# Kernel tuning notes

Measured on AMD Instinct MI355X. Metric: run time of the kernel, lower is better.

Reference implementation:

```python
import jax, jax.numpy as jnp
import numpy as np
import math

DIM = 1024
MLP = 4096
D_STATE = 16
D_CONV = 4
EXPAND = 2
D_INNER = EXPAND * DIM
HALF = D_INNER // 2
DT_RANK = math.ceil(DIM / 16)
BSZ = 2
SEQ = 2048
LN_EPS = 1e-5


def setup_inputs() -> dict:
    key = jax.random.key(0)
    ks = jax.random.split(key, 12)
    s = lambda k, shape, sc: jax.random.normal(k, shape, dtype=jnp.float32) * sc
    return {
        "x": s(ks[0], (BSZ, SEQ, DIM), 1.0),
        "ln1_g": jnp.ones((DIM,), jnp.float32),
        "ln1_b": jnp.zeros((DIM,), jnp.float32),
        "in_proj_w": s(ks[1], (D_INNER, DIM), 0.02),
        "conv_x_w": s(ks[2], (HALF, 1, D_CONV), 0.1),
        "conv_x_b": jnp.zeros((HALF,), jnp.float32),
        "conv_z_w": s(ks[3], (HALF, 1, D_CONV), 0.1),
        "conv_z_b": jnp.zeros((HALF,), jnp.float32),
        "x_proj_w": s(ks[4], (DT_RANK + 2 * D_STATE, HALF), 0.02),
        "dt_proj_w": s(ks[5], (HALF, DT_RANK), 0.02),
        "dt_proj_b": s(ks[6], (HALF,), 0.1),
        "A_log": jnp.log(jnp.tile(jnp.arange(1, D_STATE + 1, dtype=jnp.float32), (HALF, 1))),
        "Dp": jnp.ones((HALF,), jnp.float32),
        "out_proj_w": s(ks[7], (DIM, D_INNER), 0.02),
        "ln2_g": jnp.ones((DIM,), jnp.float32),
        "ln2_b": jnp.zeros((DIM,), jnp.float32),
        "mlp_w1": s(ks[8], (MLP, DIM), 0.02),
        "mlp_b1": jnp.zeros((MLP,), jnp.float32),
        "mlp_w2": s(ks[9], (DIM, MLP), 0.02),
        "mlp_b2": jnp.zeros((DIM,), jnp.float32),
    }


def _ln(x, g, b):
    mu = jnp.mean(x, -1, keepdims=True)
    v = jnp.mean((x - mu) ** 2, -1, keepdims=True)
    return (x - mu) * jax.lax.rsqrt(v + LN_EPS) * g + b


def _dwconv_same(x, w, b):
    # x: [B, C, L]; w: [C, 1, K] depthwise; PyTorch 'same' pads left=(K-1)//2, right=rest
    total = D_CONV - 1
    left = total // 2
    y = jax.lax.conv_general_dilated(
        x, w, (1,), [(left, total - left)],
        dimension_numbers=("NCH", "OIH", "NCH"),
        feature_group_count=x.shape[1])
    return y + b[None, :, None]


def _mixer(x, in_proj_w, conv_x_w, conv_x_b, conv_z_w, conv_z_b,
           x_proj_w, dt_proj_w, dt_proj_b, A_log, Dp, out_proj_w):
    Bsz = x.shape[0]
    xz = jnp.einsum('bld,ed->ble', x, in_proj_w)              # [B,L,2*HALF]
    xs, zs = jnp.split(xz, 2, axis=-1)
    xc = jax.nn.silu(_dwconv_same(jnp.swapaxes(xs, 1, 2), conv_x_w, conv_x_b))  # [B,HALF,L]
    zc = jax.nn.silu(_dwconv_same(jnp.swapaxes(zs, 1, 2), conv_z_w, conv_z_b))  # [B,HALF,L]
    u = jnp.swapaxes(xc, 1, 2)                                 # [B,L,HALF]
    x_dbl = jnp.einsum('bld,ed->ble', u, x_proj_w)             # [B,L,dt_rank+2N]
    dt, Bm, Cm = jnp.split(x_dbl, [DT_RANK, DT_RANK + D_STATE], axis=-1)
    delta = jax.nn.softplus(jnp.einsum('blr,dr->bld', dt, dt_proj_w) + dt_proj_b)  # [B,L,HALF]
    A = -jnp.exp(A_log)                                        # [HALF,N]
    dA = jnp.exp(jnp.einsum('bld,dn->lbdn', delta, A))         # [L,B,HALF,N]
    dBu = jnp.einsum('bld,bln,bld->lbdn', delta, Bm, u)        # [L,B,HALF,N]
    Cs = jnp.moveaxis(Cm, 1, 0)                                # [L,B,N]

    def step(h, t):
        dA_t, dBu_t, c_t = t
        h = dA_t * h + dBu_t                                   # [B,HALF,N]
        return h, jnp.einsum('bdn,bn->bd', h, c_t)

    h0 = jnp.zeros((Bsz, HALF, D_STATE), x.dtype)
    _, ys = jax.lax.scan(step, h0, (dA, dBu, Cs))              # ys: [L,B,HALF]
    y = jnp.moveaxis(ys, 0, 1) + u * Dp                        # [B,L,HALF]
    y = jnp.concatenate([y, jnp.swapaxes(zc, 1, 2)], axis=-1)  # [B,L,2*HALF]
    return jnp.einsum('ble,de->bld', y, out_proj_w)


def reference(x, ln1_g, ln1_b, in_proj_w, conv_x_w, conv_x_b, conv_z_w, conv_z_b,
              x_proj_w, dt_proj_w, dt_proj_b, A_log, Dp, out_proj_w,
              ln2_g, ln2_b, mlp_w1, mlp_b1, mlp_w2, mlp_b2):
    x = x + _mixer(_ln(x, ln1_g, ln1_b), in_proj_w, conv_x_w, conv_x_b,
                   conv_z_w, conv_z_b, x_proj_w, dt_proj_w, dt_proj_b,
                   A_log, Dp, out_proj_w)
    h = _ln(x, ln2_g, ln2_b)
    h = jax.nn.gelu(jnp.einsum('bld,md->blm', h, mlp_w1) + mlp_b1, approximate=False)
    h = jnp.einsum('blm,dm->bld', h, mlp_w2) + mlp_b2
    return x + h
```

## Files before the change

### kernel.cpp

```cpp
#include <hip/hip_runtime.h>
#include <math.h>

#define DIMD    1024
#define MLPD    4096
#define DSTATE  16
#define DCONV   4
#define HALF    1024
#define DINNER  2048
#define DTRANK  64
#define BSZ     2
#define SEQ     2048
#define NTOK    (BSZ*SEQ)
#define NCH     64
#define CL      (SEQ/NCH)

typedef short bf16x8 __attribute__((ext_vector_type(8)));
typedef float f32x4  __attribute__((ext_vector_type(4)));
typedef unsigned short u16;
typedef unsigned int   u32;

__device__ __forceinline__ u16 f2bf(float x) {
    union { float f; unsigned int u; } v; v.f = x;
    unsigned int r = (v.u + 0x7FFFu + ((v.u >> 16) & 1u)) >> 16;
    return (u16)r;
}
__device__ __forceinline__ float bf2f(u16 x) {
    union { unsigned int u; float f; } v; v.u = ((unsigned int)x) << 16;
    return v.f;
}

#define SZ_WIN  (DINNER*DIMD)
#define SZ_WXP  (96*HALF)
#define SZ_WDT  (HALF*DTRANK)
#define SZ_WOUT (DIMD*DINNER)
#define SZ_WM1  (MLPD*DIMD)
#define SZ_WM2  (DIMD*MLPD)
#define SZ_TOT  (SZ_WIN+SZ_WXP+SZ_WDT+SZ_WOUT+SZ_WM1+SZ_WM2)
#define CVT_BLOCKS ((SZ_TOT + 255) / 256)

__global__ __launch_bounds__(256) void cvtln_kernel(
        const float* __restrict__ x, const float* __restrict__ g,
        const float* __restrict__ b, u16* __restrict__ xn_bf,
        const float* __restrict__ s0, u16* __restrict__ d0,
        const float* __restrict__ s1, u16* __restrict__ d1,
        const float* __restrict__ s2, u16* __restrict__ d2,
        const float* __restrict__ s3, u16* __restrict__ d3,
        const float* __restrict__ s4, u16* __restrict__ d4,
        const float* __restrict__ s5, u16* __restrict__ d5) {
    if (blockIdx.x >= NTOK) {
        int i = (blockIdx.x - NTOK) * 256 + threadIdx.x;
        if (i < SZ_WIN)  { d0[i] = f2bf(s0[i]); return; }  i -= SZ_WIN;
        if (i < SZ_WXP)  { d1[i] = f2bf(s1[i]); return; }  i -= SZ_WXP;
        if (i < SZ_WDT)  { d2[i] = f2bf(s2[i]); return; }  i -= SZ_WDT;
        if (i < SZ_WOUT) { d3[i] = f2bf(s3[i]); return; }  i -= SZ_WOUT;
        if (i < SZ_WM1)  { d4[i] = f2bf(s4[i]); return; }  i -= SZ_WM1;
        if (i < SZ_WM2)  { d5[i] = f2bf(s5[i]); }
        return;
    }
    __shared__ float sm[4];
    int row = blockIdx.x;
    int t = threadIdx.x;
    const float4* xr = (const float4*)(x + (size_t)row * DIMD);
    float4 v = xr[t];
    float s = v.x + v.y + v.z + v.w;
    for (int off = 32; off > 0; off >>= 1) s += __shfl_down(s, off, 64);
    if ((t & 63) == 0) sm[t >> 6] = s;
    __syncthreads();
    float mu = (sm[0] + sm[1] + sm[2] + sm[3]) * (1.0f / DIMD);
    float dx = v.x - mu, dy = v.y - mu, dz = v.z - mu, dw = v.w - mu;
    float ss = dx*dx + dy*dy + dz*dz + dw*dw;
    for (int off = 32; off > 0; off >>= 1) ss += __shfl_down(ss, off, 64);
    __syncthreads();
    if ((t & 63) == 0) sm[t >> 6] = ss;
    __syncthreads();
    float var = (sm[0] + sm[1] + sm[2] + sm[3]) * (1.0f / DIMD);
    float rs = rsqrtf(var + 1e-5f);
    float4 gv = ((const float4*)g)[t];
    float4 bv = ((const float4*)b)[t];
    u16* o = xn_bf + (size_t)row * DIMD + t * 4;
    o[0] = f2bf(dx * rs * gv.x + bv.x);
    o[1] = f2bf(dy * rs * gv.y + bv.y);
    o[2] = f2bf(dz * rs * gv.z + bv.z);
    o[3] = f2bf(dw * rs * gv.w + bv.w);
}

__global__ __launch_bounds__(256) void gemm_small_kernel(
        const u16* __restrict__ A, int lda,
        const u16* __restrict__ W, int K, int N,
        float* __restrict__ Cf, u16* __restrict__ Cb) {
    __shared__ f32x4 red[2][64];
    int t = threadIdx.x;
    int w = t >> 6, lane = t & 63;
    int mt = w & 1, kh = w >> 1;
    int m0 = blockIdx.x * 32 + mt * 16;
    int n0 = blockIdx.y * 16;
    int r = lane & 15, quad = lane >> 4;
    int Kh = K >> 1;
    f32x4 acc = {0.f, 0.f, 0.f, 0.f};
    const u16* ap = A + (size_t)(m0 + r) * lda + kh * Kh + quad * 8;
    const u16* wp = W + (size_t)(n0 + r) * K   + kh * Kh + quad * 8;
    for (int k = 0; k < Kh; k += 32) {
        bf16x8 av = *(const bf16x8*)(ap + k);
        bf16x8 bv = *(const bf16x8*)(wp + k);
        acc = __builtin_amdgcn_mfma_f32_16x16x32_bf16(av, bv, acc, 0, 0, 0);
    }
    if (kh == 1) red[mt][lane] = acc;
    __syncthreads();
    if (kh == 0) {
        f32x4 o = red[mt][lane];
        int col = n0 + r;
        #pragma unroll
        for (int i = 0; i < 4; ++i) {
            int row = m0 + quad * 4 + i;
            size_t idx = (size_t)row * N + col;
            float v = acc[i] + o[i];
            Cf[idx] = v;
            Cb[idx] = f2bf(v);
        }
    }
}

template<int EPI, int TN, int KS>
__global__ __launch_bounds__(256) void gemm128_kernel(
        const u16* __restrict__ A, int lda, const u16* __restrict__ W,
        int K, int N,
        const float* __restrict__ bias, const float* __restrict__ resid,
        float* __restrict__ Cf, float* __restrict__ Cf2,
        u16* __restrict__ Cb) {
    constexpr int NF = TN / 32;
    __shared__ u16 As0[128 * 32], As1[128 * 32];
    __shared__ u16 Bs0[TN * 32],  Bs1[TN * 32];
    const int t = threadIdx.x;
    const int w = t >> 6;
    const int lane = t & 63;
    const int r = lane & 15, quad = lane >> 4;
    const int wm = w & 1, wn = w >> 1;
    const int m0 = blockIdx.x * 128;
    const int n0 = blockIdx.y * TN;
    const int Kloc = K / KS;
    const int kz = (KS == 2) ? blockIdx.z : 0;

    f32x4 acc[4][NF];
    #pragma unroll
    for (int mi = 0; mi < 4; ++mi)
        #pragma unroll
        for (int ni = 0; ni < NF; ++ni)
            acc[mi][ni] = (f32x4){0.f, 0.f, 0.f, 0.f};

    const u16* pa[2];
    const u16* pb[NF / 2];
    #pragma unroll
    for (int i = 0; i < 2; ++i) {
        int c = (i * 4 + w) * 64 + lane;
        int row = c >> 2;
        int q = (c & 3) ^ ((row >> 1) & 3);
        pa[i] = A + (size_t)(m0 + row) * lda + (size_t)kz * Kloc + q * 8;
    }
    #pragma unroll
    for (int i = 0; i < NF / 2; ++i) {
        int c = (i * 4 + w) * 64 + lane;
        int row = c >> 2;
        int q = (c & 3) ^ ((row >> 1) & 3);
        pb[i] = W + (size_t)(n0 + row) * K + (size_t)kz * Kloc + q * 8;
    }
    const int qs = quad ^ ((r >> 1) & 3);
    int aoff[4], boff[NF];
    #pragma unroll
    for (int mi = 0; mi < 4; ++mi)
        aoff[mi] = (wm * 64 + mi * 16 + r) * 32 + qs * 8;
    #pragma unroll
    for (int ni = 0; ni < NF; ++ni)
        boff[ni] = (wn * (TN / 2) + ni * 16 + r) * 32 + qs * 8;

    auto stage = [&](u16* __restrict__ Ad, u16* __restrict__ Bd) {
        #pragma unroll
        for (int i = 0; i < 2; ++i) {
            __builtin_amdgcn_global_load_lds(
                (const __attribute__((address_space(1))) u32*)pa[i],
                (__attribute__((address_space(3))) u32*)(Ad + (i * 4 + w) * 512),
                16, 0, 0);
            pa[i] += 32;
        }
        #pragma unroll
        for (int i = 0; i < NF / 2; ++i) {
            __builtin_amdgcn_global_load_lds(
                (const __attribute__((address_space(1))) u32*)pb[i],
                (__attribute__((address_space(3))) u32*)(Bd + (i * 4 + w) * 512),
                16, 0, 0);
            pb[i] += 32;
        }
    };
    auto compute = [&](const u16* __restrict__ Ab, const u16* __restrict__ Bb) {
        bf16x8 af[4], bfr[NF];
        #pragma unroll
        for (int mi = 0; mi < 4; ++mi) af[mi] = *(const bf16x8*)(Ab + aoff[mi]);
        #pragma unroll
        for (int ni = 0; ni < NF; ++ni) bfr[ni] = *(const bf16x8*)(Bb + boff[ni]);
        #pragma unroll
        for (int mi = 0; mi < 4; ++mi)
            #pragma unroll
            for (int ni = 0; ni < NF; ++ni)
                acc[mi][ni] = __builtin_amdgcn_mfma_f32_16x16x32_bf16(
                    af[mi], bfr[ni], acc[mi][ni], 0, 0, 0);
    };

    stage(As0, Bs0);
    for (int k0 = 0; k0 < Kloc; k0 += 64) {
        __syncthreads();
        if (k0 + 32 < Kloc) stage(As1, Bs1);
        compute(As0, Bs0);
        __syncthreads();
        if (k0 + 64 < Kloc) stage(As0, Bs0);
        compute(As1, Bs1);
    }

    float* Cfo = (KS == 2 && kz) ? Cf2 : Cf;
    #pragma unroll
    for (int mi = 0; mi < 4; ++mi) {
        #pragma unroll
        for (int i = 0; i < 4; ++i) {
            int row = m0 + wm * 64 + mi * 16 + quad * 4 + i;
            #pragma unroll
            for (int ni = 0; ni < NF; ++ni) {
                int col = n0 + wn * (TN / 2) + ni * 16 + r;
                size_t idx = (size_t)row * N + col;
                float v = acc[mi][ni][i];
                if (EPI == 1) { v += bias[col]; v = (v > 20.f) ? v : log1pf(expf(v)); }
                if (EPI == 2) {
                    v += bias[col];
                    float e = __expf(fminf(1.5957691216f * v + 0.0713548162f * v * v * v, 80.f));
                    v = v * __fdividef(e, e + 1.f);
                }
                if (EPI == 3) { v += resid[idx]; }
                if (EPI == 4) { v += bias[col] + resid[idx]; }
                if (EPI == 2 || EPI == 5) Cb[idx] = f2bf(v);
                else                      Cfo[idx] = v;
            }
        }
    }
}

__global__ __launch_bounds__(256) void reduce2_kernel(
        const float* __restrict__ P0, const float* __restrict__ P1,
        const float* __restrict__ bias, const float* __restrict__ resid,
        float* __restrict__ out) {
    size_t idx = ((size_t)blockIdx.x * 256 + threadIdx.x) * 4;
    float4 a = *(const float4*)(P0 + idx);
    float4 b = *(const float4*)(P1 + idx);
    float4 rr = *(const float4*)(resid + idx);
    int col = (int)(idx & (DIMD - 1));
    float4 bb = *(const float4*)(bias + col);
    float4 o;
    o.x = a.x + b.x + rr.x + bb.x;
    o.y = a.y + b.y + rr.y + bb.y;
    o.z = a.z + b.z + rr.z + bb.z;
    o.w = a.w + b.w + rr.w + bb.w;
    *(float4*)(out + idx) = o;
}

__global__ __launch_bounds__(256) void reduce_ln_kernel(
        const float* __restrict__ P0, const float* __restrict__ P1,
        const float* __restrict__ resid,
        const float* __restrict__ g, const float* __restrict__ b,
        float* __restrict__ x2, u16* __restrict__ out_bf) {
    __shared__ float sm[4];
    int row = blockIdx.x;
    int t = threadIdx.x;
    size_t base = (size_t)row * DIMD + t * 4;
    float4 a  = *(const float4*)(P0 + base);
    float4 p  = *(const float4*)(P1 + base);
    float4 rr = *(const float4*)(resid + base);
    float4 v;
    v.x = a.x + p.x + rr.x;
    v.y = a.y + p.y + rr.y;
    v.z = a.z + p.z + rr.z;
    v.w = a.w + p.w + rr.w;
    *(float4*)(x2 + base) = v;
    float s = v.x + v.y + v.z + v.w;
    for (int off = 32; off > 0; off >>= 1) s += __shfl_down(s, off, 64);
    if ((t & 63) == 0) sm[t >> 6] = s;
    __syncthreads();
    float mu = (sm[0] + sm[1] + sm[2] + sm[3]) * (1.0f / DIMD);
    float dx = v.x - mu, dy = v.y - mu, dz = v.z - mu, dw = v.w - mu;
    float ss = dx*dx + dy*dy + dz*dz + dw*dw;
    for (int off = 32; off > 0; off >>= 1) ss += __shfl_down(ss, off, 64);
    __syncthreads();
    if ((t & 63) == 0) sm[t >> 6] = ss;
    __syncthreads();
    float var = (sm[0] + sm[1] + sm[2] + sm[3]) * (1.0f / DIMD);
    float rs = rsqrtf(var + 1e-5f);
    float4 gv = ((const float4*)g)[t];
    float4 bv = ((const float4*)b)[t];
    u16* o = out_bf + base;
    o[0] = f2bf(dx * rs * gv.x + bv.x);
    o[1] = f2bf(dy * rs * gv.y + bv.y);
    o[2] = f2bf(dz * rs * gv.z + bv.z);
    o[3] = f2bf(dw * rs * gv.w + bv.w);
}

__global__ __launch_bounds__(256) void conv_silu_kernel(
        const u16* __restrict__ xz,
        const float* __restrict__ wx, const float* __restrict__ bx,
        const float* __restrict__ wz, const float* __restrict__ bz,
        u16* __restrict__ u_bf, u16* __restrict__ ycat) {
    int c  = blockIdx.x * 256 + threadIdx.x;
    int gy = blockIdx.y;
    int b  = gy >> 8;
    int l0 = (gy & 255) * 8;
    const u16* base = xz + ((size_t)(b * SEQ + l0)) * DINNER;
    float wxr[4], wzr[4];
    #pragma unroll
    for (int k = 0; k < 4; ++k) { wxr[k] = wx[c * 4 + k]; wzr[k] = wz[c * 4 + k]; }
    float bxv = bx[c], bzv = bz[c];
    float xm1 = (l0 > 0) ? bf2f(base[c - DINNER]) : 0.f;
    float x0v = bf2f(base[c]);
    float x1v = bf2f(base[c + DINNER]);
    float zm1 = (l0 > 0) ? bf2f(base[HALF + c - DINNER]) : 0.f;
    float z0v = bf2f(base[HALF + c]);
    float z1v = bf2f(base[HALF + c + DINNER]);
    u16* up = u_bf + ((size_t)(b * SEQ + l0)) * HALF + c;
    u16* yp = ycat + ((size_t)(b * SEQ + l0)) * DINNER + HALF + c;
    #pragma unroll
    for (int l = 0; l < 8; ++l) {
        bool in = (l0 + l + 2) < SEQ;
        float x2v = in ? bf2f(base[(size_t)(l + 2) * DINNER + c]) : 0.f;
        float z2v = in ? bf2f(base[(size_t)(l + 2) * DINNER + HALF + c]) : 0.f;
        float ax = bxv + wxr[0]*xm1 + wxr[1]*x0v + wxr[2]*x1v + wxr[3]*x2v;
        float az = bzv + wzr[0]*zm1 + wzr[1]*z0v + wzr[2]*z1v + wzr[3]*z2v;
        float sx = ax * __fdividef(1.f, 1.f + __expf(-ax));
        float sz = az * __fdividef(1.f, 1.f + __expf(-az));
        *up = f2bf(sx); *yp = f2bf(sz);
        up += HALF; yp += DINNER;
        xm1 = x0v; x0v = x1v; x1v = x2v;
        zm1 = z0v; z0v = z1v; z1v = z2v;
    }
}

__global__ __launch_bounds__(256) void scan_p1_kernel(
        const float* __restrict__ delta, const u16* __restrict__ u_bf,
        const float* __restrict__ x_dbl, const float* __restrict__ A_log,
        float* __restrict__ hfin, float* __restrict__ dsum) {
    int t  = blockIdx.x * 256 + threadIdx.x;
    int d  = t & (HALF - 1);
    int ch = (t >> 10) & (NCH - 1);
    int b  = t >> 16;
    float Ac[16], h[16];
    #pragma unroll
    for (int i = 0; i < 4; ++i) {
        float4 a = *(const float4*)&A_log[d * DSTATE + i * 4];
        Ac[4*i+0] = -__expf(a.x); Ac[4*i+1] = -__expf(a.y);
        Ac[4*i+2] = -__expf(a.z); Ac[4*i+3] = -__expf(a.w);
        h[4*i+0] = 0.f; h[4*i+1] = 0.f; h[4*i+2] = 0.f; h[4*i+3] = 0.f;
    }
    int l0 = b * SEQ + ch * CL;
    size_t off = (size_t)l0 * HALF + d;
    const float* xrow = x_dbl + (size_t)l0 * 96;
    float ds = 0.f;
    #pragma unroll 4
    for (int l = 0; l < CL; ++l) {
        float dl = delta[off];
        float uv = bf2f(u_bf[off]);
        off += HALF;
        float4 B0 = *(const float4*)(xrow + 64);
        float4 B1 = *(const float4*)(xrow + 68);
        float4 B2 = *(const float4*)(xrow + 72);
        float4 B3 = *(const float4*)(xrow + 76);
        xrow += 96;
        float dBu = dl * uv;
        ds += dl;
        float Bv[16] = {B0.x,B0.y,B0.z,B0.w, B1.x,B1.y,B1.z,B1.w,
                        B2.x,B2.y,B2.z,B2.w, B3.x,B3.y,B3.z,B3.w};
        #pragma unroll
        for (int n = 0; n < 16; ++n)
            h[n] = __expf(dl * Ac[n]) * h[n] + dBu * Bv[n];
    }
    float4* hf = (float4*)&hfin[(size_t)t * 16];
    #pragma unroll
    for (int i = 0; i < 4; ++i)
        hf[i] = (float4){h[4*i+0], h[4*i+1], h[4*i+2], h[4*i+3]};
    dsum[t] = ds;
}

__global__ __launch_bounds__(256) void scan_p2_kernel(
        const float* __restrict__ A_log, const float* __restrict__ dsum,
        const float* __restrict__ hfin, float* __restrict__ hin) {
    int t = blockIdx.x * 256 + threadIdx.x;
    int n = t & 15;
    int d = (t >> 4) & (HALF - 1);
    int b = t >> 14;
    float Ac = -__expf(A_log[d * DSTATE + n]);
    float h = 0.f;
    for (int ch = 0; ch < NCH; ++ch) {
        size_t chain = ((size_t)(b * NCH + ch) * HALF) + d;
        hin[chain * 16 + n] = h;
        float ds = dsum[chain];
        h = __expf(Ac * ds) * h + hfin[chain * 16 + n];
    }
}

__global__ __launch_bounds__(256) void scan_p3_kernel(
        const float* __restrict__ delta, const u16* __restrict__ u_bf,
        const float* __restrict__ x_dbl, const float* __restrict__ A_log,
        const float* __restrict__ Dp, const float* __restrict__ hin,
        u16* __restrict__ ycat) {
    int t  = blockIdx.x * 256 + threadIdx.x;
    int d  = t & (HALF - 1);
    int ch = (t >> 10) & (NCH - 1);
    int b  = t >> 16;
    float Ac[16], h[16];
    #pragma unroll
    for (int i = 0; i < 4; ++i) {
        float4 a  = *(const float4*)&A_log[d * DSTATE + i * 4];
        float4 hv = *(const float4*)&hin[(size_t)t * 16 + i * 4];
        Ac[4*i+0] = -__expf(a.x); Ac[4*i+1] = -__expf(a.y);
        Ac[4*i+2] = -__expf(a.z); Ac[4*i+3] = -__expf(a.w);
        h[4*i+0] = hv.x; h[4*i+1] = hv.y; h[4*i+2] = hv.z; h[4*i+3] = hv.w;
    }
    float Dv = Dp[d];
    int l0 = b * SEQ + ch * CL;
    size_t off = (size_t)l0 * HALF + d;
    const float* xrow = x_dbl + (size_t)l0 * 96;
    u16* yp = ycat + (size_t)l0 * DINNER + d;
    #pragma unroll 4
    for (int l = 0; l < CL; ++l) {
        float dl = delta[off];
        float uv = bf2f(u_bf[off]);
        off += HALF;
        float4 B0 = *(const float4*)(xrow + 64);
        float4 B1 = *(const float4*)(xrow + 68);
        float4 B2 = *(const float4*)(xrow + 72);
        float4 B3 = *(const float4*)(xrow + 76);
        float4 C0 = *(const float4*)(xrow + 80);
        float4 C1 = *(const float4*)(xrow + 84);
        float4 C2 = *(const float4*)(xrow + 88);
        float4 C3 = *(const float4*)(xrow + 92);
        xrow += 96;
        float dBu = dl * uv;
        float Bv[16] = {B0.x,B0.y,B0.z,B0.w, B1.x,B1.y,B1.z,B1.w,
                        B2.x,B2.y,B2.z,B2.w, B3.x,B3.y,B3.z,B3.w};
        float Cv[16] = {C0.x,C0.y,C0.z,C0.w, C1.x,C1.y,C1.z,C1.w,
                        C2.x,C2.y,C2.z,C2.w, C3.x,C3.y,C3.z,C3.w};
        float y = uv * Dv;
        #pragma unroll
        for (int n = 0; n < 16; ++n) {
            h[n] = __expf(dl * Ac[n]) * h[n] + dBu * Bv[n];
            y += h[n] * Cv[n];
        }
        *yp = f2bf(y);
        yp += DINNER;
    }
}

extern "C" void kernel_launch(void* const* d_in, const int* in_sizes, int n_in,
                              void* d_out, int out_size, void* d_ws, size_t ws_size,
                              hipStream_t stream) {
    const float* x         = (const float*)d_in[0];
    const float* ln1_g     = (const float*)d_in[1];
    const float* ln1_b     = (const float*)d_in[2];
    const float* in_proj_w = (const float*)d_in[3];
    const float* conv_x_w  = (const float*)d_in[4];
    const float* conv_x_b  = (const float*)d_in[5];
    const float* conv_z_w  = (const float*)d_in[6];
    const float* conv_z_b  = (const float*)d_in[7];
    const float* x_proj_w  = (const float*)d_in[8];
    const float* dt_proj_w = (const float*)d_in[9];
    const float* dt_proj_b = (const float*)d_in[10];
    const float* A_log     = (const float*)d_in[11];
    const float* Dp        = (const float*)d_in[12];
    const float* out_proj_w= (const float*)d_in[13];
    const float* ln2_g     = (const float*)d_in[14];
    const float* ln2_b     = (const float*)d_in[15];
    const float* mlp_w1    = (const float*)d_in[16];
    const float* mlp_b1    = (const float*)d_in[17];
    const float* mlp_w2    = (const float*)d_in[18];
    const float* mlp_b2    = (const float*)d_in[19];
    float* out = (float*)d_out;

    char* p = (char*)d_ws;
    auto alloc = [&](size_t bytes) {
        char* r = p; p += (bytes + 255) & ~(size_t)255; return r;
    };
    u16*   w_in   = (u16*)  alloc((size_t)DINNER * DIMD * 2);
    u16*   w_xp   = (u16*)  alloc((size_t)96 * HALF * 2);
    u16*   w_dt   = (u16*)  alloc((size_t)HALF * DTRANK * 2);
    u16*   w_out  = (u16*)  alloc((size_t)DIMD * DINNER * 2);
    u16*   w_m1   = (u16*)  alloc((size_t)MLPD * DIMD * 2);
    u16*   w_m2   = (u16*)  alloc((size_t)DIMD * MLPD * 2);
    u16*   xn_bf  = (u16*)  alloc((size_t)NTOK * DIMD * 2);
    u16*   xz_bf  = (u16*)  alloc((size_t)NTOK * DINNER * 2);
    u16*   u_bf   = (u16*)  alloc((size_t)NTOK * HALF * 2);
    u16*   ycat   = (u16*)  alloc((size_t)NTOK * DINNER * 2);
    float* x_dbl  = (float*)alloc((size_t)NTOK * 96 * 4);
    u16*   xdbl_bf= (u16*)  alloc((size_t)NTOK * 96 * 2);
    float* delta  = (float*)alloc((size_t)NTOK * HALF * 4);
    float* x2     = (float*)alloc((size_t)NTOK * DIMD * 4);
    u16*   ln2_bf = (u16*)  alloc((size_t)NTOK * DIMD * 2);
    u16*   mlp_h  = (u16*)  alloc((size_t)NTOK * MLPD * 2);
    float* hfin = (float*)mlp_h;
    float* hin  = hfin + (size_t)BSZ * NCH * HALF * DSTATE;
    float* dsum = hin  + (size_t)BSZ * NCH * HALF * DSTATE;
    float* P0 = delta;
    float* P1 = (float*)xz_bf;

    cvtln_kernel<<<NTOK + CVT_BLOCKS, 256, 0, stream>>>(
        x, ln1_g, ln1_b, xn_bf,
        in_proj_w, w_in, x_proj_w, w_xp, dt_proj_w, w_dt,
        out_proj_w, w_out, mlp_w1, w_m1, mlp_w2, w_m2);

    gemm128_kernel<5,64,1><<<dim3(NTOK/128, DINNER/64), 256, 0, stream>>>(
        xn_bf, DIMD, w_in, DIMD, DINNER, nullptr, nullptr, nullptr, nullptr, xz_bf);

    conv_silu_kernel<<<dim3(HALF/256, NTOK/8), 256, 0, stream>>>(
        xz_bf, conv_x_w, conv_x_b, conv_z_w, conv_z_b, u_bf, ycat);

    gemm_small_kernel<<<dim3(NTOK/32, 96/16), 256, 0, stream>>>(
        u_bf, HALF, w_xp, HALF, 96, x_dbl, xdbl_bf);

    gemm128_kernel<1,64,1><<<dim3(NTOK/128, HALF/64), 256, 0, stream>>>(
        xdbl_bf, 96, w_dt, DTRANK, HALF, dt_proj_b, nullptr, delta, nullptr, nullptr);

    scan_p1_kernel<<<(BSZ*NCH*HALF)/256, 256, 0, stream>>>(
        delta, u_bf, x_dbl, A_log, hfin, dsum);
    scan_p2_kernel<<<(BSZ*HALF*DSTATE)/256, 256, 0, stream>>>(
        A_log, dsum, hfin, hin);
    scan_p3_kernel<<<(BSZ*NCH*HALF)/256, 256, 0, stream>>>(
        delta, u_bf, x_dbl, A_log, Dp, hin, ycat);

    gemm128_kernel<0,64,2><<<dim3(NTOK/128, DIMD/64, 2), 256, 0, stream>>>(
        ycat, DINNER, w_out, DINNER, DIMD, nullptr, nullptr, P0, P1, nullptr);
    reduce_ln_kernel<<<NTOK, 256, 0, stream>>>(
        P0, P1, x, ln2_g, ln2_b, x2, ln2_bf);

    gemm128_kernel<2,128,1><<<dim3(NTOK/128, MLPD/128), 256, 0, stream>>>(
        ln2_bf, DIMD, w_m1, DIMD, MLPD, mlp_b1, nullptr, nullptr, nullptr, mlp_h);

    gemm128_kernel<0,64,2><<<dim3(NTOK/128, DIMD/64, 2), 256, 0, stream>>>(
        mlp_h, MLPD, w_m2, MLPD, DIMD, nullptr, nullptr, P0, P1, nullptr);
    reduce2_kernel<<<(NTOK*DIMD)/1024, 256, 0, stream>>>(
        P0, P1, mlp_b2, x2, out);
}
```

Before: 443.9 us.

## Load A fragments directly to registers in GEMM, share B tile across warps

The 128-row GEMM no longer stages the A tile through shared memory. Each warp now owns 32 rows and loads its A fragments straight from global memory into registers with a one-step prefetch, while the whole B tile goes through LDS and every warp reads all of it. The goal is to cut LDS traffic and staging for A and to drop the A shared buffers. The MLP-up GEMM also moves from a 128-wide to a 64-wide N tile. The cost is less reuse of B across warps and uncoalesced global A reads of 16-byte pieces per row, which may raise global load pressure.

After: 516.7 us. +16.4%, slower.

```diff
diff --git a/kernel.cpp b/kernel.cpp
--- a/kernel.cpp
+++ b/kernel.cpp
@@ -127,62 +127,47 @@
         const float* __restrict__ bias, const float* __restrict__ resid,
         float* __restrict__ Cf, float* __restrict__ Cf2,
         u16* __restrict__ Cb) {
-    constexpr int NF = TN / 32;
-    __shared__ u16 As0[128 * 32], As1[128 * 32];
-    __shared__ u16 Bs0[TN * 32],  Bs1[TN * 32];
+    constexpr int NW = TN / 16;
+    constexpr int NB = TN * 4 / 256;
+    __shared__ u16 Bs0[TN * 32], Bs1[TN * 32];
     const int t = threadIdx.x;
     const int w = t >> 6;
     const int lane = t & 63;
     const int r = lane & 15, quad = lane >> 4;
-    const int wm = w & 1, wn = w >> 1;
     const int m0 = blockIdx.x * 128;
     const int n0 = blockIdx.y * TN;
     const int Kloc = K / KS;
     const int kz = (KS == 2) ? blockIdx.z : 0;
 
-    f32x4 acc[4][NF];
-    #pragma unroll
-    for (int mi = 0; mi < 4; ++mi)
-        #pragma unroll
-        for (int ni = 0; ni < NF; ++ni)
+    f32x4 acc[2][NW];
+    #pragma unroll
+    for (int mi = 0; mi < 2; ++mi)
+        #pragma unroll
+        for (int ni = 0; ni < NW; ++ni)
             acc[mi][ni] = (f32x4){0.f, 0.f, 0.f, 0.f};
 
-    const u16* pa[2];
-    const u16* pb[NF / 2];
-    #pragma unroll
-    for (int i = 0; i < 2; ++i) {
-        int c = (i * 4 + w) * 64 + lane;
-        int row = c >> 2;
-        int q = (c & 3) ^ ((row >> 1) & 3);
-        pa[i] = A + (size_t)(m0 + row) * lda + (size_t)kz * Kloc + q * 8;
-    }
-    #pragma unroll
-    for (int i = 0; i < NF / 2; ++i) {
+    const u16* pA[2];
+    #pragma unroll
+    for (int mi = 0; mi < 2; ++mi)
+        pA[mi] = A + (size_t)(m0 + w * 32 + mi * 16 + r) * lda
+                   + (size_t)kz * Kloc + quad * 8;
+    const u16* pb[NB];
+    #pragma unroll
+    for (int i = 0; i < NB; ++i) {
         int c = (i * 4 + w) * 64 + lane;
         int row = c >> 2;
         int q = (c & 3) ^ ((row >> 1) & 3);
         pb[i] = W + (size_t)(n0 + row) * K + (size_t)kz * Kloc + q * 8;
     }
     const int qs = quad ^ ((r >> 1) & 3);
-    int aoff[4], boff[NF];
-    #pragma unroll
-    for (int mi = 0; mi < 4; ++mi)
-        aoff[mi] = (wm * 64 + mi * 16 + r) * 32 + qs * 8;
-    #pragma unroll
-    for (int ni = 0; ni < NF; ++ni)
-        boff[ni] = (wn * (TN / 2) + ni * 16 + r) * 32 + qs * 8;
-
-    auto stage = [&](u16* __restrict__ Ad, u16* __restrict__ Bd) {
-        #pragma unroll
-        for (int i = 0; i < 2; ++i) {
-            __builtin_amdgcn_global_load_lds(
-                (const __attribute__((address_space(1))) u32*)pa[i],
-                (__attribute__((address_space(3))) u32*)(Ad + (i * 4 + w) * 512),
-                16, 0, 0);
-            pa[i] += 32;
-        }
-        #pragma unroll
-        for (int i = 0; i < NF / 2; ++i) {
+    int boff[NW];
+    #pragma unroll
+    for (int ni = 0; ni < NW; ++ni)
+        boff[ni] = (ni * 16 + r) * 32 + qs * 8;
+
+    auto stageB = [&](u16* __restrict__ Bd) {
+        #pragma unroll
+        for (int i = 0; i < NB; ++i) {
             __builtin_amdgcn_global_load_lds(
                 (const __attribute__((address_space(1))) u32*)pb[i],
                 (__attribute__((address_space(3))) u32*)(Bd + (i * 4 + w) * 512),
@@ -190,39 +175,46 @@
             pb[i] += 32;
         }
     };
-    auto compute = [&](const u16* __restrict__ Ab, const u16* __restrict__ Bb) {
-        bf16x8 af[4], bfr[NF];
-        #pragma unroll
-        for (int mi = 0; mi < 4; ++mi) af[mi] = *(const bf16x8*)(Ab + aoff[mi]);
-        #pragma unroll
-        for (int ni = 0; ni < NF; ++ni) bfr[ni] = *(const bf16x8*)(Bb + boff[ni]);
-        #pragma unroll
-        for (int mi = 0; mi < 4; ++mi)
+    auto loadA = [&](bf16x8* dst) {
+        #pragma unroll
+        for (int mi = 0; mi < 2; ++mi) {
+            dst[mi] = *(const bf16x8*)pA[mi];
+            pA[mi] += 32;
+        }
+    };
+    auto compute = [&](const bf16x8* a, const u16* __restrict__ Bb) {
+        bf16x8 bfr[NW];
+        #pragma unroll
+        for (int ni = 0; ni < NW; ++ni) bfr[ni] = *(const bf16x8*)(Bb + boff[ni]);
+        #pragma unroll
+        for (int mi = 0; mi < 2; ++mi)
             #pragma unroll
-            for (int ni = 0; ni < NF; ++ni)
+            for (int ni = 0; ni < NW; ++ni)
                 acc[mi][ni] = __builtin_amdgcn_mfma_f32_16x16x32_bf16(
-                    af[mi], bfr[ni], acc[mi][ni], 0, 0, 0);
+                    a[mi], bfr[ni], acc[mi][ni], 0, 0, 0);
     };
 
-    stage(As0, Bs0);
+    bf16x8 aC[2], aN[2];
+    stageB(Bs0);
+    loadA(aC);
     for (int k0 = 0; k0 < Kloc; k0 += 64) {
         __syncthreads();
-        if (k0 + 32 < Kloc) stage(As1, Bs1);
-        compute(As0, Bs0);
+        if (k0 + 32 < Kloc) { stageB(Bs1); loadA(aN); }
+        compute(aC, Bs0);
         __syncthreads();
-        if (k0 + 64 < Kloc) stage(As0, Bs0);
-        compute(As1, Bs1);
+        if (k0 + 64 < Kloc) { stageB(Bs0); loadA(aC); }
+        compute(aN, Bs1);
     }
 
     float* Cfo = (KS == 2 && kz) ? Cf2 : Cf;
     #pragma unroll
-    for (int mi = 0; mi < 4; ++mi) {
+    for (int mi = 0; mi < 2; ++mi) {
         #pragma unroll
         for (int i = 0; i < 4; ++i) {
-            int row = m0 + wm * 64 + mi * 16 + quad * 4 + i;
+            int row = m0 + w * 32 + mi * 16 + quad * 4 + i;
             #pragma unroll
-            for (int ni = 0; ni < NF; ++ni) {
-                int col = n0 + wn * (TN / 2) + ni * 16 + r;
+            for (int ni = 0; ni < NW; ++ni) {
+                int col = n0 + ni * 16 + r;
                 size_t idx = (size_t)row * N + col;
                 float v = acc[mi][ni][i];
                 if (EPI == 1) { v += bias[col]; v = (v > 20.f) ? v : log1pf(expf(v)); }
@@ -531,7 +523,7 @@
     reduce_ln_kernel<<<NTOK, 256, 0, stream>>>(
         P0, P1, x, ln2_g, ln2_b, x2, ln2_bf);
 
-    gemm128_kernel<2,128,1><<<dim3(NTOK/128, MLPD/128), 256, 0, stream>>>(
+    gemm128_kernel<2,64,1><<<dim3(NTOK/128, MLPD/64), 256, 0, stream>>>(
         ln2_bf, DIMD, w_m1, DIMD, MLPD, mlp_b1, nullptr, nullptr, nullptr, mlp_h);
 
     gemm128_kernel<0,64,2><<<dim3(NTOK/128, DIMD/64, 2), 256, 0, stream>>>(
```

## Raise split-K to four for output GEMMs and add dedicated dt_proj kernel

Applied to the files above, without the earlier changes.

The out_proj and MLP-down GEMMs now split K four ways instead of two. Each GEMM writes four fp32 partial buffers, and the reduce and reduce+LayerNorm kernels sum all four. Some partials are placed in reused scratch buffers, plus one new buffer. The dt_proj GEMM (K=64) gets a small dedicated MFMA kernel with a fused softplus instead of the general 128-tile kernel. The aim is more blocks in flight for the long-K GEMMs and less tile overhead on the tiny-K GEMM, at the cost of extra partial-sum memory traffic.

Result: slower. 453.1 us (+2.1%).

```diff
diff --git a/kernel.cpp b/kernel.cpp
--- a/kernel.cpp
+++ b/kernel.cpp
@@ -120,12 +120,43 @@
     }
 }
 
+__global__ __launch_bounds__(256) void gemm_k64_kernel(
+        const u16* __restrict__ A, int lda,
+        const u16* __restrict__ W, int N,
+        const float* __restrict__ bias, float* __restrict__ Cf) {
+    int t = threadIdx.x;
+    int w = t >> 6, lane = t & 63;
+    int mt = w & 1, nt = w >> 1;
+    int m0 = blockIdx.x * 32 + mt * 16;
+    int n0 = blockIdx.y * 32 + nt * 16;
+    int r = lane & 15, quad = lane >> 4;
+    const u16* ap = A + (size_t)(m0 + r) * lda + quad * 8;
+    const u16* wp = W + (size_t)(n0 + r) * DTRANK + quad * 8;
+    bf16x8 a0 = *(const bf16x8*)ap;
+    bf16x8 a1 = *(const bf16x8*)(ap + 32);
+    bf16x8 b0 = *(const bf16x8*)wp;
+    bf16x8 b1 = *(const bf16x8*)(wp + 32);
+    f32x4 acc = {0.f, 0.f, 0.f, 0.f};
+    acc = __builtin_amdgcn_mfma_f32_16x16x32_bf16(a0, b0, acc, 0, 0, 0);
+    acc = __builtin_amdgcn_mfma_f32_16x16x32_bf16(a1, b1, acc, 0, 0, 0);
+    int col = n0 + r;
+    float bv = bias[col];
+    #pragma unroll
+    for (int i = 0; i < 4; ++i) {
+        int row = m0 + quad * 4 + i;
+        float v = acc[i] + bv;
+        v = (v > 20.f) ? v : log1pf(expf(v));
+        Cf[(size_t)row * N + col] = v;
+    }
+}
+
 template<int EPI, int TN, int KS>
 __global__ __launch_bounds__(256) void gemm128_kernel(
         const u16* __restrict__ A, int lda, const u16* __restrict__ W,
         int K, int N,
-        const float* __restrict__ bias, const float* __restrict__ resid,
-        float* __restrict__ Cf, float* __restrict__ Cf2,
+        const float* __restrict__ bias,
+        float* __restrict__ C0, float* __restrict__ C1,
+        float* __restrict__ C2, float* __restrict__ C3,
         u16* __restrict__ Cb) {
     constexpr int NF = TN / 32;
     __shared__ u16 As0[128 * 32], As1[128 * 32];
@@ -138,7 +169,7 @@
     const int m0 = blockIdx.x * 128;
     const int n0 = blockIdx.y * TN;
     const int Kloc = K / KS;
-    const int kz = (KS == 2) ? blockIdx.z : 0;
+    const int kz = (KS > 1) ? blockIdx.z : 0;
 
     f32x4 acc[4][NF];
     #pragma unroll
@@ -214,7 +245,7 @@
         compute(As1, Bs1);
     }
 
-    float* Cfo = (KS == 2 && kz) ? Cf2 : Cf;
+    float* Cfo = (kz == 0) ? C0 : (kz == 1) ? C1 : (kz == 2) ? C2 : C3;
     #pragma unroll
     for (int mi = 0; mi < 4; ++mi) {
         #pragma unroll
@@ -225,14 +256,11 @@
                 int col = n0 + wn * (TN / 2) + ni * 16 + r;
                 size_t idx = (size_t)row * N + col;
                 float v = acc[mi][ni][i];
-                if (EPI == 1) { v += bias[col]; v = (v > 20.f) ? v : log1pf(expf(v)); }
                 if (EPI == 2) {
                     v += bias[col];
                     float e = __expf(fminf(1.5957691216f * v + 0.0713548162f * v * v * v, 80.f));
                     v = v * __fdividef(e, e + 1.f);
                 }
-                if (EPI == 3) { v += resid[idx]; }
-                if (EPI == 4) { v += bias[col] + resid[idx]; }
                 if (EPI == 2 || EPI == 5) Cb[idx] = f2bf(v);
                 else                      Cfo[idx] = v;
             }
@@ -240,26 +268,30 @@
     }
 }
 
-__global__ __launch_bounds__(256) void reduce2_kernel(
+__global__ __launch_bounds__(256) void reduce4_kernel(
         const float* __restrict__ P0, const float* __restrict__ P1,
+        const float* __restrict__ P2, const float* __restrict__ P3,
         const float* __restrict__ bias, const float* __restrict__ resid,
         float* __restrict__ out) {
     size_t idx = ((size_t)blockIdx.x * 256 + threadIdx.x) * 4;
     float4 a = *(const float4*)(P0 + idx);
     float4 b = *(const float4*)(P1 + idx);
+    float4 c = *(const float4*)(P2 + idx);
+    float4 d = *(const float4*)(P3 + idx);
     float4 rr = *(const float4*)(resid + idx);
     int col = (int)(idx & (DIMD - 1));
     float4 bb = *(const float4*)(bias + col);
     float4 o;
-    o.x = a.x + b.x + rr.x + bb.x;
-    o.y = a.y + b.y + rr.y + bb.y;
-    o.z = a.z + b.z + rr.z + bb.z;
-    o.w = a.w + b.w + rr.w + bb.w;
+    o.x = a.x + b.x + c.x + d.x + rr.x + bb.x;
+    o.y = a.y + b.y + c.y + d.y + rr.y + bb.y;
+    o.z = a.z + b.z + c.z + d.z + rr.z + bb.z;
+    o.w = a.w + b.w + c.w + d.w + rr.w + bb.w;
     *(float4*)(out + idx) = o;
 }
 
-__global__ __launch_bounds__(256) void reduce_ln_kernel(
+__global__ __launch_bounds__(256) void reduce_ln4_kernel(
         const float* __restrict__ P0, const float* __restrict__ P1,
+        const float* __restrict__ P2, const float* __restrict__ P3,
         const float* __restrict__ resid,
         const float* __restrict__ g, const float* __restrict__ b,
         float* __restrict__ x2, u16* __restrict__ out_bf) {
@@ -269,12 +301,14 @@
     size_t base = (size_t)row * DIMD + t * 4;
     float4 a  = *(const float4*)(P0 + base);
     float4 p  = *(const float4*)(P1 + base);
+    float4 c  = *(const float4*)(P2 + base);
+    float4 d  = *(const float4*)(P3 + base);
     float4 rr = *(const float4*)(resid + base);
     float4 v;
-    v.x = a.x + p.x + rr.x;
-    v.y = a.y + p.y + rr.y;
-    v.z = a.z + p.z + rr.z;
-    v.w = a.w + p.w + rr.w;
+    v.x = a.x + p.x + c.x + d.x + rr.x;
+    v.y = a.y + p.y + c.y + d.y + rr.y;
+    v.z = a.z + p.z + c.z + d.z + rr.z;
+    v.w = a.w + p.w + c.w + d.w + rr.w;
     *(float4*)(x2 + base) = v;
     float s = v.x + v.y + v.z + v.w;
     for (int off = 32; off > 0; off >>= 1) s += __shfl_down(s, off, 64);
@@ -496,11 +530,16 @@
     float* x2     = (float*)alloc((size_t)NTOK * DIMD * 4);
     u16*   ln2_bf = (u16*)  alloc((size_t)NTOK * DIMD * 2);
     u16*   mlp_h  = (u16*)  alloc((size_t)NTOK * MLPD * 2);
+    float* Px     = (float*)alloc((size_t)NTOK * DIMD * 4);
     float* hfin = (float*)mlp_h;
     float* hin  = hfin + (size_t)BSZ * NCH * HALF * DSTATE;
     float* dsum = hin  + (size_t)BSZ * NCH * HALF * DSTATE;
     float* P0 = delta;
     float* P1 = (float*)xz_bf;
+    float* P2o = (float*)mlp_h;
+    float* P3o = (float*)mlp_h + (size_t)NTOK * DIMD;
+    float* P2m = (float*)ycat;
+    float* P3m = Px;
 
     cvtln_kernel<<<NTOK + CVT_BLOCKS, 256, 0, stream>>>(
         x, ln1_g, ln1_b, xn_bf,
@@ -508,7 +547,8 @@
         out_proj_w, w_out, mlp_w1, w_m1, mlp_w2, w_m2);
 
     gemm128_kernel<5,64,1><<<dim3(NTOK/128, DINNER/64), 256, 0, stream>>>(
-        xn_bf, DIMD, w_in, DIMD, DINNER, nullptr, nullptr, nullptr, nullptr, xz_bf);
+        xn_bf, DIMD, w_in, DIMD, DINNER, nullptr,
+        nullptr, nullptr, nullptr, nullptr, xz_bf);
 
     conv_silu_kernel<<<dim3(HALF/256, NTOK/8), 256, 0, stream>>>(
         xz_bf, conv_x_w, conv_x_b, conv_z_w, conv_z_b, u_bf, ycat);
@@ -516,8 +556,8 @@
     gemm_small_kernel<<<dim3(NTOK/32, 96/16), 256, 0, stream>>>(
         u_bf, HALF, w_xp, HALF, 96, x_dbl, xdbl_bf);
 
-    gemm128_kernel<1,64,1><<<dim3(NTOK/128, HALF/64), 256, 0, stream>>>(
-        xdbl_bf, 96, w_dt, DTRANK, HALF, dt_proj_b, nullptr, delta, nullptr, nullptr);
+    gemm_k64_kernel<<<dim3(NTOK/32, HALF/32), 256, 0, stream>>>(
+        xdbl_bf, 96, w_dt, HALF, dt_proj_b, delta);
 
     scan_p1_kernel<<<(BSZ*NCH*HALF)/256, 256, 0, stream>>>(
         delta, u_bf, x_dbl, A_log, hfin, dsum);
@@ -526,16 +566,19 @@
     scan_p3_kernel<<<(BSZ*NCH*HALF)/256, 256, 0, stream>>>(
         delta, u_bf, x_dbl, A_log, Dp, hin, ycat);
 
-    gemm128_kernel<0,64,2><<<dim3(NTOK/128, DIMD/64, 2), 256, 0, stream>>>(
-        ycat, DINNER, w_out, DINNER, DIMD, nullptr, nullptr, P0, P1, nullptr);
-    reduce_ln_kernel<<<NTOK, 256, 0, stream>>>(
-        P0, P1, x, ln2_g, ln2_b, x2, ln2_bf);
+    gemm128_kernel<0,64,4><<<dim3(NTOK/128, DIMD/64, 4), 256, 0, stream>>>(
+        ycat, DINNER, w_out, DINNER, DIMD, nullptr,
+        P0, P1, P2o, P3o, nullptr);
+    reduce_ln4_kernel<<<NTOK, 256, 0, stream>>>(
+        P0, P1, P2o, P3o, x, ln2_g, ln2_b, x2, ln2_bf);
 
     gemm128_kernel<2,128,1><<<dim3(NTOK/128, MLPD/128), 256, 0, stream>>>(
-        ln2_bf, DIMD, w_m1, DIMD, MLPD, mlp_b1, nullptr, nullptr, nullptr, mlp_h);
-
-    gemm128_kernel<0,64,2><<<dim3(NTOK/128, DIMD/64, 2), 256, 0, stream>>>(
-        mlp_h, MLPD, w_m2, MLPD, DIMD, nullptr, nullptr, P0, P1, nullptr);
-    reduce2_kernel<<<(NTOK*DIMD)/1024, 256, 0, stream>>>(
-        P0, P1, mlp_b2, x2, out);
-}
+        ln2_bf, DIMD, w_m1, DIMD, MLPD, mlp_b1,
+        nullptr, nullptr, nullptr, nullptr, mlp_h);
+
+    gemm128_kernel<0,64,4><<<dim3(NTOK/128, DIMD/64, 4), 256, 0, stream>>>(
+        mlp_h, MLPD, w_m2, MLPD, DIMD, nullptr,
+        P0, P1, P2m, P3m, nullptr);
+    reduce4_kernel<<<(NTOK*DIMD)/1024, 256, 0, stream>>>(
+        P0, P1, P2m, P3m, mlp_b2, x2, out);
+}
```
